# Optimization experiments

Measured on AMD Instinct MI355X. Metric: run time of the kernel, lower is better.

Reference implementation:

```python
import jax, jax.numpy as jnp
import numpy as np

E, T, I, O = 8, 8192, 2048, 4096  # experts, total_tokens, in_features, out_features


def setup_inputs() -> dict:
    key = jax.random.key(0)
    k1, k2, k3 = jax.random.split(key, 3)
    inputs = jax.random.normal(k1, (T, I), dtype=jnp.float32)
    # lecun_normal-style scale for the (E, I, O) kernel (fan_in = I)
    kernel = jax.random.normal(k2, (E, I, O), dtype=jnp.float32) * (1.0 / np.float32(np.sqrt(I)))
    # nonzero bias so the ragged bias-expansion path is exercised
    bias = jax.random.normal(k3, (E, O), dtype=jnp.float32) * 0.02
    # tokens are sorted by expert; equal groups summing exactly to T
    group_sizes = jnp.full((E,), T // E, dtype=jnp.int32)
    return {"inputs": inputs, "group_sizes": group_sizes, "kernel": kernel, "bias": bias}


def reference(inputs, group_sizes, kernel, bias):
    # Ragged grouped GEMM: row block g of `inputs` (size group_sizes[g]) is
    # multiplied by kernel[g] of shape (I, O). Matches _ragged_dot with
    # out_first=False: contraction dims ((1,), (1,)), rhs group dim 0.
    out = jax.lax.ragged_dot(inputs, kernel, group_sizes)  # (T, O)
    # Per-group bias add: bias[e] broadcast over that expert's token block.
    expert_ids = jnp.repeat(jnp.arange(E), group_sizes, total_repeat_length=T)
    return out + bias[expert_ids]
```

## Files before the change

kernel.cpp:

```cpp
#include <hip/hip_runtime.h>


typedef short bf16x8 __attribute__((ext_vector_type(8)));
typedef float f32x4 __attribute__((ext_vector_type(4)));
typedef unsigned short u16x8 __attribute__((ext_vector_type(8)));

constexpr int Ecnt = 8;
constexpr int Ttok = 8192;
constexpr int Ifeat = 2048;
constexpr int Ofeat = 4096;
constexpr int BM = 128, BN = 128, BK = 64;
constexpr int NTILE = (Ttok / BM) * (Ofeat / BN);
constexpr int QCAP = NTILE / 8;

__device__ __forceinline__ unsigned short f2bf(float f) {
  unsigned u = __float_as_uint(f);
  unsigned r = (u + 0x7FFFu + ((u >> 16) & 1u)) >> 16;
  return (unsigned short)r;
}

__global__ __launch_bounds__(256) void cvt_a(const float* __restrict__ src,
                                             unsigned short* __restrict__ dst) {
  size_t i = ((size_t)blockIdx.x * 256 + threadIdx.x) * 8;
  float4 f0 = *(const float4*)(src + i);
  float4 f1 = *(const float4*)(src + i + 4);
  u16x8 v;
  v[0] = f2bf(f0.x); v[1] = f2bf(f0.y); v[2] = f2bf(f0.z); v[3] = f2bf(f0.w);
  v[4] = f2bf(f1.x); v[5] = f2bf(f1.y); v[6] = f2bf(f1.z); v[7] = f2bf(f1.w);
  *(u16x8*)(dst + i) = v;
}

__global__ __launch_bounds__(256) void cvt_b(const float* __restrict__ src,
                                             unsigned short* __restrict__ dst) {
  constexpr int LDST = 129;
  __shared__ float tile[64 * LDST];
  const int e = blockIdx.z;
  const int i0 = blockIdx.y * 64;
  const int o0 = blockIdx.x * 128;
  const int tid = threadIdx.x;
  {
    const int tx = tid & 31, ty = tid >> 5;
    const float* s = src + ((size_t)e * Ifeat + i0) * Ofeat + o0 + tx * 4;
#pragma unroll
    for (int r = 0; r < 8; ++r) {
      int i = r * 8 + ty;
      float4 f = *(const float4*)(s + (size_t)i * Ofeat);
      float* l = tile + i * LDST + tx * 4;
      l[0] = f.x; l[1] = f.y; l[2] = f.z; l[3] = f.w;
    }
  }
  __syncthreads();
  {
    const int ic = (tid & 7) * 8;
    const int oc = tid >> 3;
#pragma unroll
    for (int p = 0; p < 4; ++p) {
      int o = p * 32 + oc;
      u16x8 v;
#pragma unroll
      for (int j = 0; j < 8; ++j) v[j] = f2bf(tile[(ic + j) * LDST + o]);
      unsigned short* d =
          dst + ((size_t)e * Ofeat + o0 + o) * Ifeat + i0 + ic;
      *(u16x8*)d = v;
    }
  }
}

__device__ __forceinline__ void ld16(const unsigned short* g, unsigned short* l) {
  __builtin_amdgcn_global_load_lds(
      (const __attribute__((address_space(1))) unsigned int*)g,
      (__attribute__((address_space(3))) unsigned int*)l, 16, 0, 0);
}

__global__ __launch_bounds__(256) void moe_gemm(
    const unsigned short* __restrict__ A,
    const unsigned short* __restrict__ Bt,
    const int* __restrict__ gs,
    const float* __restrict__ bias,
    float* __restrict__ C,
    int* __restrict__ qcnt) {
  __shared__ unsigned short lA[BM * BK];
  __shared__ unsigned short lB[BN * BK];
  __shared__ int s_tile;

  const int tid = threadIdx.x;

  if (tid == 0) {
    unsigned xcc = __builtin_amdgcn_s_getreg(63508) & 7;
    int t = 0;
#pragma unroll
    for (int a = 0; a < 8; ++a) {
      int q = (xcc + a) & 7;
      int idx = atomicAdd(&qcnt[q], 1);
      if (idx < QCAP) { t = (q << 8) | idx; break; }
    }
    s_tile = t;
  }
  __syncthreads();

  const int tcode = s_tile;
  const int q = tcode >> 8;
  const int idx = tcode & 255;
  const int rt = q * 8 + (idx & 7);
  const int ct = idx >> 3;
  const int row0 = rt * BM;
  const int col0 = ct * BN;

  int e = 0;
  {
    int cum = 0;
#pragma unroll
    for (int g = 0; g < Ecnt; ++g) {
      int s = gs[g];
      if (row0 >= cum + s) { cum += s; e = g + 1; }
    }
  }

  const unsigned short* Ag = A + (size_t)row0 * Ifeat;
  const unsigned short* Bg = Bt + ((size_t)e * Ofeat + col0) * Ifeat;

  const int wave = tid >> 6, lane = tid & 63;
  const int wm = (wave >> 1) * 64, wn = (wave & 1) * 64;
  const int lrow = lane & 15;
  const int kg = lane >> 4;
  const int xr = lrow & 7;

  const int64_t koff[4] = {
      (int64_t)((tid + 0) >> 3) * Ifeat + (((tid + 0) & 7) ^ (((tid + 0) >> 3) & 7)) * 8,
      (int64_t)((tid + 256) >> 3) * Ifeat + (((tid + 256) & 7) ^ (((tid + 256) >> 3) & 7)) * 8,
      (int64_t)((tid + 512) >> 3) * Ifeat + (((tid + 512) & 7) ^ (((tid + 512) >> 3) & 7)) * 8,
      (int64_t)((tid + 768) >> 3) * Ifeat + (((tid + 768) & 7) ^ (((tid + 768) >> 3) & 7)) * 8};
  const unsigned short* asrc[4] = {Ag + koff[0], Ag + koff[1], Ag + koff[2],
                                   Ag + koff[3]};
  const unsigned short* bsrc[4] = {Bg + koff[0], Bg + koff[1], Bg + koff[2],
                                   Bg + koff[3]};
  unsigned short* adst[4] = {lA + (size_t)tid * 8, lA + (size_t)(tid + 256) * 8,
                             lA + (size_t)(tid + 512) * 8,
                             lA + (size_t)(tid + 768) * 8};
  unsigned short* bdst[4] = {lB + (size_t)tid * 8, lB + (size_t)(tid + 256) * 8,
                             lB + (size_t)(tid + 512) * 8,
                             lB + (size_t)(tid + 768) * 8};

  f32x4 acc[4][4];
#pragma unroll
  for (int i = 0; i < 4; ++i)
#pragma unroll
    for (int jj = 0; jj < 4; ++jj) acc[i][jj] = (f32x4){0.f, 0.f, 0.f, 0.f};

  for (int k0 = 0; k0 < Ifeat; k0 += BK) {
#pragma unroll
    for (int p = 0; p < 4; ++p) ld16(asrc[p] + k0, adst[p]);
#pragma unroll
    for (int p = 0; p < 4; ++p) ld16(bsrc[p] + k0, bdst[p]);
    __syncthreads();

#pragma unroll
    for (int s = 0; s < 2; ++s) {
      bf16x8 af[4], bf[4];
#pragma unroll
      for (int mt = 0; mt < 4; ++mt) {
        const int r = wm + mt * 16 + lrow;
        const int slot = (s * 4 + kg) ^ xr;
        af[mt] = *(const bf16x8*)(lA + r * BK + slot * 8);
      }
#pragma unroll
      for (int nt = 0; nt < 4; ++nt) {
        const int r = wn + nt * 16 + lrow;
        const int slot = (s * 4 + kg) ^ xr;
        bf[nt] = *(const bf16x8*)(lB + r * BK + slot * 8);
      }
#pragma unroll
      for (int mt = 0; mt < 4; ++mt)
#pragma unroll
        for (int nt = 0; nt < 4; ++nt)
          acc[mt][nt] = __builtin_amdgcn_mfma_f32_16x16x32_bf16(
              af[mt], bf[nt], acc[mt][nt], 0, 0, 0);
    }

    __syncthreads();
  }

  const int r0 = (lane >> 4) * 4;
  const int cc = lane & 15;
  const float* be = bias + (size_t)e * Ofeat;
#pragma unroll
  for (int mt = 0; mt < 4; ++mt) {
    const int row = row0 + wm + mt * 16 + r0;
#pragma unroll
    for (int nt = 0; nt < 4; ++nt) {
      const int col = col0 + wn + nt * 16 + cc;
      const float b = be[col];
      float* Cp = C + (size_t)row * Ofeat + col;
#pragma unroll
      for (int r = 0; r < 4; ++r) Cp[(size_t)r * Ofeat] = acc[mt][nt][r] + b;
    }
  }
}

extern "C" void kernel_launch(void* const* d_in, const int* in_sizes, int n_in,
                              void* d_out, int out_size, void* d_ws, size_t ws_size,
                              hipStream_t stream) {
  const float* inputs = (const float*)d_in[0];
  const int* group_sizes = (const int*)d_in[1];
  const float* kern = (const float*)d_in[2];
  const float* bias = (const float*)d_in[3];
  float* out = (float*)d_out;

  unsigned short* Abf = (unsigned short*)d_ws;
  unsigned short* Bbf = Abf + (size_t)Ttok * Ifeat;
  const size_t cnt_off = (size_t)Ttok * Ifeat * 2 + (size_t)Ecnt * Ofeat * Ifeat * 2;
  int* qcnt = (int*)((char*)d_ws + cnt_off);

  cvt_a<<<(Ttok * (size_t)Ifeat) / (8 * 256), 256, 0, stream>>>(inputs, Abf);
  cvt_b<<<dim3(Ofeat / 128, Ifeat / 64, Ecnt), 256, 0, stream>>>(kern, Bbf);
  hipMemsetAsync(qcnt, 0, 8 * sizeof(int), stream);

  moe_gemm<<<NTILE, 256, 0, stream>>>(Abf, Bbf, group_sizes, bias, out, qcnt);
}
```

Before: 629.6 us.

## Use 256x256 tiles with double-buffered LDS prefetch and fuse counter reset

Enlarges the GEMM block tile to 256x256 with 512 threads and double-buffers LDS so the next K-slice loads while MFMAs run, with barriers and priority hints interleaving loads and compute. Tile assignment now maps each queue to one expert's row range. The counter memset is folded into the input conversion kernel, which now converts four elements per thread. The larger LDS footprint limits occupancy and the per-queue mapping assumes equal group sizes.

```diff
diff --git a/kernel.cpp b/kernel.cpp
--- a/kernel.cpp
+++ b/kernel.cpp
@@ -3,14 +3,19 @@
 
 typedef short bf16x8 __attribute__((ext_vector_type(8)));
 typedef float f32x4 __attribute__((ext_vector_type(4)));
+typedef unsigned short u16x4 __attribute__((ext_vector_type(4)));
 typedef unsigned short u16x8 __attribute__((ext_vector_type(8)));
 
 constexpr int Ecnt = 8;
 constexpr int Ttok = 8192;
 constexpr int Ifeat = 2048;
 constexpr int Ofeat = 4096;
-constexpr int BM = 128, BN = 128, BK = 64;
-constexpr int NTILE = (Ttok / BM) * (Ofeat / BN);
+
+constexpr int BM = 256, BN = 256, BK = 64;
+constexpr int NKT = Ifeat / BK;
+constexpr int RTE = (Ttok / Ecnt) / BM;
+constexpr int CTN = Ofeat / BN;
+constexpr int NTILE = Ecnt * RTE * CTN;
 constexpr int QCAP = NTILE / 8;
 
 __device__ __forceinline__ unsigned short f2bf(float f) {
@@ -20,14 +25,14 @@
 }
 
 __global__ __launch_bounds__(256) void cvt_a(const float* __restrict__ src,
-                                             unsigned short* __restrict__ dst) {
-  size_t i = ((size_t)blockIdx.x * 256 + threadIdx.x) * 8;
-  float4 f0 = *(const float4*)(src + i);
-  float4 f1 = *(const float4*)(src + i + 4);
-  u16x8 v;
-  v[0] = f2bf(f0.x); v[1] = f2bf(f0.y); v[2] = f2bf(f0.z); v[3] = f2bf(f0.w);
-  v[4] = f2bf(f1.x); v[5] = f2bf(f1.y); v[6] = f2bf(f1.z); v[7] = f2bf(f1.w);
-  *(u16x8*)(dst + i) = v;
+                                             unsigned short* __restrict__ dst,
+                                             int* __restrict__ qcnt) {
+  size_t i = ((size_t)blockIdx.x * 256 + threadIdx.x) * 4;
+  float4 f = *(const float4*)(src + i);
+  u16x4 v;
+  v[0] = f2bf(f.x); v[1] = f2bf(f.y); v[2] = f2bf(f.z); v[3] = f2bf(f.w);
+  *(u16x4*)(dst + i) = v;
+  if (blockIdx.x == 0 && threadIdx.x < 8) qcnt[threadIdx.x] = 0;
 }
 
 __global__ __launch_bounds__(256) void cvt_b(const float* __restrict__ src,
@@ -72,15 +77,15 @@
       (__attribute__((address_space(3))) unsigned int*)l, 16, 0, 0);
 }
 
-__global__ __launch_bounds__(256) void moe_gemm(
+__global__ __launch_bounds__(512, 2) void moe_gemm(
     const unsigned short* __restrict__ A,
     const unsigned short* __restrict__ Bt,
     const int* __restrict__ gs,
     const float* __restrict__ bias,
     float* __restrict__ C,
     int* __restrict__ qcnt) {
-  __shared__ unsigned short lA[BM * BK];
-  __shared__ unsigned short lB[BN * BK];
+  __shared__ unsigned short lA[2][BM * BK];
+  __shared__ unsigned short lB[2][BN * BK];
   __shared__ int s_tile;
 
   const int tid = threadIdx.x;
@@ -90,20 +95,20 @@
     int t = 0;
 #pragma unroll
     for (int a = 0; a < 8; ++a) {
-      int q = (xcc + a) & 7;
-      int idx = atomicAdd(&qcnt[q], 1);
-      if (idx < QCAP) { t = (q << 8) | idx; break; }
+      int qq = (xcc + a) & 7;
+      int ix = atomicAdd(&qcnt[qq], 1);
+      if (ix < QCAP) { t = (qq << 6) | ix; break; }
     }
     s_tile = t;
   }
   __syncthreads();
 
   const int tcode = s_tile;
-  const int q = tcode >> 8;
-  const int idx = tcode & 255;
-  const int rt = q * 8 + (idx & 7);
-  const int ct = idx >> 3;
-  const int row0 = rt * BM;
+  const int q = tcode >> 6;
+  const int idx = tcode & 63;
+  const int rt = idx & (RTE - 1);
+  const int ct = idx >> 2;
+  const int row0 = q * (Ttok / Ecnt) + rt * BM;
   const int col0 = ct * BN;
 
   int e = 0;
@@ -116,79 +121,123 @@
     }
   }
 
-  const unsigned short* Ag = A + (size_t)row0 * Ifeat;
-  const unsigned short* Bg = Bt + ((size_t)e * Ofeat + col0) * Ifeat;
+  const unsigned short* __restrict__ Ag = A + (size_t)row0 * Ifeat;
+  const unsigned short* __restrict__ Bg = Bt + ((size_t)e * Ofeat + col0) * Ifeat;
+
+  int64_t goff[4];
+  int lof[4];
+#pragma unroll
+  for (int p = 0; p < 4; ++p) {
+    const int c = tid + p * 512;
+    const int r = c >> 3, kcp = c & 7;
+    goff[p] = (int64_t)r * Ifeat + ((kcp ^ (r & 7)) << 3);
+    lof[p] = c << 3;
+  }
 
   const int wave = tid >> 6, lane = tid & 63;
-  const int wm = (wave >> 1) * 64, wn = (wave & 1) * 64;
+  const int wr = wave >> 2, wc = wave & 3;
   const int lrow = lane & 15;
   const int kg = lane >> 4;
   const int xr = lrow & 7;
-
-  const int64_t koff[4] = {
-      (int64_t)((tid + 0) >> 3) * Ifeat + (((tid + 0) & 7) ^ (((tid + 0) >> 3) & 7)) * 8,
-      (int64_t)((tid + 256) >> 3) * Ifeat + (((tid + 256) & 7) ^ (((tid + 256) >> 3) & 7)) * 8,
-      (int64_t)((tid + 512) >> 3) * Ifeat + (((tid + 512) & 7) ^ (((tid + 512) >> 3) & 7)) * 8,
-      (int64_t)((tid + 768) >> 3) * Ifeat + (((tid + 768) & 7) ^ (((tid + 768) >> 3) & 7)) * 8};
-  const unsigned short* asrc[4] = {Ag + koff[0], Ag + koff[1], Ag + koff[2],
-                                   Ag + koff[3]};
-  const unsigned short* bsrc[4] = {Bg + koff[0], Bg + koff[1], Bg + koff[2],
-                                   Bg + koff[3]};
-  unsigned short* adst[4] = {lA + (size_t)tid * 8, lA + (size_t)(tid + 256) * 8,
-                             lA + (size_t)(tid + 512) * 8,
-                             lA + (size_t)(tid + 768) * 8};
-  unsigned short* bdst[4] = {lB + (size_t)tid * 8, lB + (size_t)(tid + 256) * 8,
-                             lB + (size_t)(tid + 512) * 8,
-                             lB + (size_t)(tid + 768) * 8};
-
-  f32x4 acc[4][4];
-#pragma unroll
-  for (int i = 0; i < 4; ++i)
+  const int aslot0 = (kg ^ xr) << 3;
+  const int aslot1 = ((4 + kg) ^ xr) << 3;
+  const int arbase = (wr * 128 + lrow) * BK;
+  const int brbase = (wc * 64 + lrow) * BK;
+
+  f32x4 acc[8][4];
+#pragma unroll
+  for (int i = 0; i < 8; ++i)
 #pragma unroll
     for (int jj = 0; jj < 4; ++jj) acc[i][jj] = (f32x4){0.f, 0.f, 0.f, 0.f};
 
-  for (int k0 = 0; k0 < Ifeat; k0 += BK) {
-#pragma unroll
-    for (int p = 0; p < 4; ++p) ld16(asrc[p] + k0, adst[p]);
-#pragma unroll
-    for (int p = 0; p < 4; ++p) ld16(bsrc[p] + k0, bdst[p]);
+#pragma unroll
+  for (int p = 0; p < 4; ++p) ld16(Ag + goff[p], &lA[0][lof[p]]);
+#pragma unroll
+  for (int p = 0; p < 4; ++p) ld16(Bg + goff[p], &lB[0][lof[p]]);
+  __syncthreads();
+
+#define AFRAG(MT, SL) (*(const bf16x8*)(al + arbase + (MT) * (16 * BK) + (SL)))
+#define MFMA_QUAD(MT0, MT1)                                                  \
+  __builtin_amdgcn_s_barrier();                                              \
+  __builtin_amdgcn_s_setprio(1);                                             \
+  _Pragma("unroll") for (int nt = 0; nt < 4; ++nt) {                         \
+    acc[MT0][nt] = __builtin_amdgcn_mfma_f32_16x16x32_bf16(                  \
+        a00, bf[nt][0], acc[MT0][nt], 0, 0, 0);                              \
+    acc[MT0][nt] = __builtin_amdgcn_mfma_f32_16x16x32_bf16(                  \
+        a01, bf[nt][1], acc[MT0][nt], 0, 0, 0);                              \
+    acc[MT1][nt] = __builtin_amdgcn_mfma_f32_16x16x32_bf16(                  \
+        a10, bf[nt][0], acc[MT1][nt], 0, 0, 0);                              \
+    acc[MT1][nt] = __builtin_amdgcn_mfma_f32_16x16x32_bf16(                  \
+        a11, bf[nt][1], acc[MT1][nt], 0, 0, 0);                              \
+  }                                                                          \
+  __builtin_amdgcn_s_setprio(0);
+
+  int cur = 0;
+  for (int kt = 0; kt < NKT; ++kt) {
+    const unsigned short* al = lA[cur];
+    const unsigned short* bl = lB[cur];
+    unsigned short* an = lA[cur ^ 1];
+    unsigned short* bn = lB[cur ^ 1];
+    const int64_t kn = (int64_t)(kt + 1) * BK;
+    const bool pf = (kt + 1 < NKT);
+
+    bf16x8 bf[4][2];
+#pragma unroll
+    for (int nt = 0; nt < 4; ++nt) {
+      bf[nt][0] = *(const bf16x8*)(bl + brbase + nt * (16 * BK) + aslot0);
+      bf[nt][1] = *(const bf16x8*)(bl + brbase + nt * (16 * BK) + aslot1);
+    }
+
+    {
+      bf16x8 a00 = AFRAG(0, aslot0), a01 = AFRAG(0, aslot1);
+      bf16x8 a10 = AFRAG(1, aslot0), a11 = AFRAG(1, aslot1);
+      if (pf) {
+        ld16(Ag + goff[0] + kn, an + lof[0]);
+        ld16(Ag + goff[1] + kn, an + lof[1]);
+        ld16(Ag + goff[2] + kn, an + lof[2]);
+        ld16(Ag + goff[3] + kn, an + lof[3]);
+      }
+      MFMA_QUAD(0, 1)
+      __builtin_amdgcn_s_barrier();
+    }
+    {
+      bf16x8 a00 = AFRAG(2, aslot0), a01 = AFRAG(2, aslot1);
+      bf16x8 a10 = AFRAG(3, aslot0), a11 = AFRAG(3, aslot1);
+      if (pf) {
+        ld16(Bg + goff[0] + kn, bn + lof[0]);
+        ld16(Bg + goff[1] + kn, bn + lof[1]);
+        ld16(Bg + goff[2] + kn, bn + lof[2]);
+        ld16(Bg + goff[3] + kn, bn + lof[3]);
+      }
+      MFMA_QUAD(2, 3)
+      __builtin_amdgcn_s_barrier();
+    }
+    {
+      bf16x8 a00 = AFRAG(4, aslot0), a01 = AFRAG(4, aslot1);
+      bf16x8 a10 = AFRAG(5, aslot0), a11 = AFRAG(5, aslot1);
+      MFMA_QUAD(4, 5)
+      __builtin_amdgcn_s_barrier();
+    }
+    {
+      bf16x8 a00 = AFRAG(6, aslot0), a01 = AFRAG(6, aslot1);
+      bf16x8 a10 = AFRAG(7, aslot0), a11 = AFRAG(7, aslot1);
+      MFMA_QUAD(6, 7)
+    }
     __syncthreads();
-
-#pragma unroll
-    for (int s = 0; s < 2; ++s) {
-      bf16x8 af[4], bf[4];
-#pragma unroll
-      for (int mt = 0; mt < 4; ++mt) {
-        const int r = wm + mt * 16 + lrow;
-        const int slot = (s * 4 + kg) ^ xr;
-        af[mt] = *(const bf16x8*)(lA + r * BK + slot * 8);
-      }
-#pragma unroll
-      for (int nt = 0; nt < 4; ++nt) {
-        const int r = wn + nt * 16 + lrow;
-        const int slot = (s * 4 + kg) ^ xr;
-        bf[nt] = *(const bf16x8*)(lB + r * BK + slot * 8);
-      }
-#pragma unroll
-      for (int mt = 0; mt < 4; ++mt)
-#pragma unroll
-        for (int nt = 0; nt < 4; ++nt)
-          acc[mt][nt] = __builtin_amdgcn_mfma_f32_16x16x32_bf16(
-              af[mt], bf[nt], acc[mt][nt], 0, 0, 0);
-    }
-
-    __syncthreads();
-  }
+    cur ^= 1;
+  }
+#undef AFRAG
+#undef MFMA_QUAD
 
   const int r0 = (lane >> 4) * 4;
   const int cc = lane & 15;
   const float* be = bias + (size_t)e * Ofeat;
 #pragma unroll
-  for (int mt = 0; mt < 4; ++mt) {
-    const int row = row0 + wm + mt * 16 + r0;
+  for (int mt = 0; mt < 8; ++mt) {
+    const int row = row0 + wr * 128 + mt * 16 + r0;
 #pragma unroll
     for (int nt = 0; nt < 4; ++nt) {
-      const int col = col0 + wn + nt * 16 + cc;
+      const int col = col0 + wc * 64 + nt * 16 + cc;
       const float b = be[col];
       float* Cp = C + (size_t)row * Ofeat + col;
 #pragma unroll
@@ -211,9 +260,8 @@
   const size_t cnt_off = (size_t)Ttok * Ifeat * 2 + (size_t)Ecnt * Ofeat * Ifeat * 2;
   int* qcnt = (int*)((char*)d_ws + cnt_off);
 
-  cvt_a<<<(Ttok * (size_t)Ifeat) / (8 * 256), 256, 0, stream>>>(inputs, Abf);
+  cvt_a<<<(Ttok * (size_t)Ifeat) / (4 * 256), 256, 0, stream>>>(inputs, Abf, qcnt);
   cvt_b<<<dim3(Ofeat / 128, Ifeat / 64, Ecnt), 256, 0, stream>>>(kern, Bbf);
-  hipMemsetAsync(qcnt, 0, 8 * sizeof(int), stream);
-
-  moe_gemm<<<NTILE, 256, 0, stream>>>(Abf, Bbf, group_sizes, bias, out, qcnt);
-}
+
+  moe_gemm<<<NTILE, 512, 0, stream>>>(Abf, Bbf, group_sizes, bias, out, qcnt);
+}
```

After: 623.2 us. Within noise of the previous version (-1.0%).
